# Kernel tuning notes

Hardware: AMD Instinct MI355X
Metric: run time of the kernel (lower is better)

Reference implementation:

```python
import jax, jax.numpy as jnp
import numpy as np

B, S, E, DK = 8, 2048, 1024, 64


def setup_inputs() -> dict:
    key = jax.random.key(0)
    ks = jax.random.split(key, 10)
    inv_e = 1.0 / np.sqrt(E)
    return {
        "k": jax.random.normal(ks[0], (B, S, E), dtype=jnp.float32),
        "q": jax.random.normal(ks[1], (B, S, E), dtype=jnp.float32),
        "v": jax.random.normal(ks[2], (B, S, E), dtype=jnp.float32),
        "mask": jax.random.randint(ks[3], (B, S, S), 0, 2, dtype=jnp.int32),
        "w_q": jax.random.uniform(ks[4], (DK, E), jnp.float32, -inv_e, inv_e),
        "b_q": jax.random.uniform(ks[5], (DK,), jnp.float32, -inv_e, inv_e),
        "w_k": jax.random.uniform(ks[6], (DK, E), jnp.float32, -inv_e, inv_e),
        "b_k": jax.random.uniform(ks[7], (DK,), jnp.float32, -inv_e, inv_e),
        "w_v": jax.random.uniform(ks[8], (DK, E), jnp.float32, -inv_e, inv_e),
        "b_v": jax.random.uniform(ks[9], (DK,), jnp.float32, -inv_e, inv_e),
    }


def reference(k, q, v, mask, w_q, b_q, w_k, b_k, w_v, b_v):
    # Linear projections: x @ W^T + b  -> [B, S, DK]
    K = jnp.einsum('bse,de->bsd', k, w_k) + b_k
    Q = jnp.einsum('bse,de->bsd', q, w_q) + b_q
    V = jnp.einsum('bse,de->bsd', v, w_v) + b_v
    scale = 1.0 / jnp.sqrt(jnp.asarray(DK, dtype=Q.dtype))
    scores = jnp.einsum('bqd,bkd->bqk', Q, K) * scale  # [B, S, S]
    scores = jnp.where(mask == 0, jnp.asarray(-1e9, scores.dtype), scores)
    attention_weights = jax.nn.softmax(scores, axis=2)
    attention_scores = jnp.einsum('bqk,bkd->bqd', attention_weights, V)
    return attention_scores, attention_weights
```

## Files before the change

### kernel.cpp

```cpp
#include <hip/hip_runtime.h>
#include <math.h>
#include <stdint.h>

#define BB 8
#define SS 2048
#define EE 1024
#define DKK 64

typedef _Float16 half8 __attribute__((ext_vector_type(8)));
typedef float floatx4 __attribute__((ext_vector_type(4)));

__device__ __forceinline__ half8 cvt8(float4 a, float4 b) {
  half8 h;
  h[0] = (_Float16)a.x; h[1] = (_Float16)a.y; h[2] = (_Float16)a.z; h[3] = (_Float16)a.w;
  h[4] = (_Float16)b.x; h[5] = (_Float16)b.y; h[6] = (_Float16)b.z; h[7] = (_Float16)b.w;
  return h;
}

__device__ __forceinline__ void split8(float4 a, float4 b, half8& hi, half8& lo) {
  float va[8] = {a.x, a.y, a.z, a.w, b.x, b.y, b.z, b.w};
#pragma unroll
  for (int j = 0; j < 8; ++j) {
    _Float16 h = (_Float16)va[j];
    hi[j] = h;
    lo[j] = (_Float16)(va[j] - (float)h);
  }
}

__global__ __launch_bounds__(256, 3) void proj_kernel(
    const float* __restrict__ q_in, const float* __restrict__ k_in,
    const float* __restrict__ v_in,
    const float* __restrict__ w_q, const float* __restrict__ b_q,
    const float* __restrict__ w_k, const float* __restrict__ b_k,
    const float* __restrict__ w_v, const float* __restrict__ b_v,
    float* __restrict__ Qp, float* __restrict__ Kp, float* __restrict__ VpT) {
  const int which = blockIdx.y;
  const float* X = which == 0 ? q_in : (which == 1 ? k_in : v_in);
  const float* W = which == 0 ? w_q : (which == 1 ? w_k : w_v);
  const float* bias = which == 0 ? b_q : (which == 1 ? b_k : b_v);

  __shared__ __align__(16) char Xh[64 * 128];
  __shared__ __align__(16) char Xl[64 * 128];
  __shared__ __align__(16) char Wh[64 * 128];
  __shared__ __align__(16) char Wl[64 * 128];

  const int t = threadIdx.x;
  const int row0 = blockIdx.x * 64;
  const int sr = t >> 2;
  const int c4 = t & 3;
  const int l = t & 63;
  const int li = l & 15, g = l >> 4;
  const int w = t >> 6;

  const float* xbase = X + (size_t)(row0 + sr) * EE + c4 * 16;
  const float* wbase = W + (size_t)sr * EE + c4 * 16;

  float4 xr[4], wr[4];
#pragma unroll
  for (int u = 0; u < 4; ++u) {
    xr[u] = ((const float4*)xbase)[u];
    wr[u] = ((const float4*)wbase)[u];
  }

  floatx4 acc[4];
#pragma unroll
  for (int c = 0; c < 4; ++c) acc[c] = (floatx4){0.f, 0.f, 0.f, 0.f};

  const int xrow_off = (w * 16 + li) * 128;
  const int swz = li & 7;

  for (int e0 = 0; e0 < EE; e0 += 64) {
    half8 xh0, xl0, xh1, xl1, wh0, wl0, wh1, wl1;
    split8(xr[0], xr[1], xh0, xl0);
    split8(xr[2], xr[3], xh1, xl1);
    split8(wr[0], wr[1], wh0, wl0);
    split8(wr[2], wr[3], wh1, wl1);
    __syncthreads();
    {
      const int p0 = ((c4 * 2 + 0) ^ (sr & 7)) * 16;
      const int p1 = ((c4 * 2 + 1) ^ (sr & 7)) * 16;
      *(half8*)(Xh + sr * 128 + p0) = xh0;
      *(half8*)(Xh + sr * 128 + p1) = xh1;
      *(half8*)(Xl + sr * 128 + p0) = xl0;
      *(half8*)(Xl + sr * 128 + p1) = xl1;
      *(half8*)(Wh + sr * 128 + p0) = wh0;
      *(half8*)(Wh + sr * 128 + p1) = wh1;
      *(half8*)(Wl + sr * 128 + p0) = wl0;
      *(half8*)(Wl + sr * 128 + p1) = wl1;
    }
    if (e0 + 64 < EE) {
#pragma unroll
      for (int u = 0; u < 4; ++u) {
        xr[u] = ((const float4*)(xbase + e0 + 64))[u];
        wr[u] = ((const float4*)(wbase + e0 + 64))[u];
      }
    }
    __syncthreads();
    half8 axh[2], axl[2];
#pragma unroll
    for (int h = 0; h < 2; ++h) {
      const int apos = ((h * 4 + g) ^ swz) * 16;
      axh[h] = *(const half8*)(Xh + xrow_off + apos);
      axl[h] = *(const half8*)(Xl + xrow_off + apos);
    }
#pragma unroll
    for (int c = 0; c < 4; ++c) {
      const int brow_off = (c * 16 + li) * 128;
#pragma unroll
      for (int h = 0; h < 2; ++h) {
        const int bpos = ((h * 4 + g) ^ swz) * 16;
        half8 bh = *(const half8*)(Wh + brow_off + bpos);
        half8 bl = *(const half8*)(Wl + brow_off + bpos);
        acc[c] = __builtin_amdgcn_mfma_f32_16x16x32_f16(axh[h], bh, acc[c], 0, 0, 0);
        acc[c] = __builtin_amdgcn_mfma_f32_16x16x32_f16(axh[h], bl, acc[c], 0, 0, 0);
        acc[c] = __builtin_amdgcn_mfma_f32_16x16x32_f16(axl[h], bh, acc[c], 0, 0, 0);
      }
    }
  }

  float bvv[4];
#pragma unroll
  for (int c = 0; c < 4; ++c) bvv[c] = bias[c * 16 + li];

  if (which < 2) {
    float* P = (which == 0) ? Qp : Kp;
#pragma unroll
    for (int c = 0; c < 4; ++c)
#pragma unroll
      for (int r = 0; r < 4; ++r)
        P[(size_t)(row0 + w * 16 + g * 4 + r) * DKK + c * 16 + li] = acc[c][r] + bvv[c];
  } else {
    const int bb = row0 >> 11;
    const int s0 = row0 & (SS - 1);
#pragma unroll
    for (int c = 0; c < 4; ++c)
#pragma unroll
      for (int r = 0; r < 4; ++r)
        VpT[((size_t)bb * DKK + c * 16 + li) * SS + s0 + w * 16 + g * 4 + r] =
            acc[c][r] + bvv[c];
  }
}

__global__ __launch_bounds__(512, 4) void attn_kernel(
    const float* __restrict__ Qp, const float* __restrict__ Kp,
    const float* __restrict__ VpT, const int* __restrict__ mask,
    float* __restrict__ outsc, float* __restrict__ wts) {
  __shared__ __align__(16) char Kraw[128 * 128];
  __shared__ __align__(16) char Vraw[64 * 256];
  __shared__ __align__(16) char Praw[2 * 16 * 272];
  __shared__ uint32_t mbits[512][5];
  __shared__ float mlb[2][4][16][2];

  const int t = threadIdx.x;
  const int b = blockIdx.x & 7;
  const int q0 = (blockIdx.x >> 3) * 32;
  const int l = t & 63;
  const int g = l >> 4, li = l & 15;
  const int w = t >> 6;
  const int qhalf = w & 1, cq = w >> 1;
  const float SCALE = 0.125f;

  half8 aq[2];
  {
    const float* qptr = Qp + ((size_t)b * SS + q0 + qhalf * 16 + li) * DKK;
#pragma unroll
    for (int h = 0; h < 2; ++h) {
      float4 a = *(const float4*)(qptr + h * 32 + g * 8);
      float4 c4 = *(const float4*)(qptr + h * 32 + g * 8 + 4);
      aq[h] = cvt8(a, c4);
    }
  }

  float m_r[4], l_r[4], rl_r[4];
#pragma unroll
  for (int r = 0; r < 4; ++r) { m_r[r] = -3.0e38f; l_r[r] = 0.f; }
#pragma unroll
  for (int i = 0; i < 4; ++i) mbits[t][i] = 0;

  const size_t qrow0 = (size_t)b * SS + q0 + qhalf * 16 + g * 4;

  for (int kt = 0; kt < 16; ++kt) {
    __syncthreads();
    {
      const int kr = t >> 3, c = t & 7;
#pragma unroll
      for (int p = 0; p < 2; ++p) {
        const int kk = kr + p * 64;
        const float* src = Kp + ((size_t)b * SS + (size_t)kt * 128 + kk) * DKK + c * 8;
        float4 a = ((const float4*)src)[0];
        float4 d4 = ((const float4*)src)[1];
        *(half8*)(Kraw + kk * 128 + ((c ^ (kk & 7)) * 16)) = cvt8(a, d4);
      }
    }
    __syncthreads();
    floatx4 sc[2];
#pragma unroll
    for (int cb2 = 0; cb2 < 2; ++cb2) {
      const int krow = (cq * 2 + cb2) * 16 + li;
      floatx4 acc = {0.f, 0.f, 0.f, 0.f};
#pragma unroll
      for (int h = 0; h < 2; ++h) {
        half8 bk = *(const half8*)(Kraw + krow * 128 + (((h * 4 + g) ^ (li & 7)) * 16));
        acc = __builtin_amdgcn_mfma_f32_16x16x32_f16(aq[h], bk, acc, 0, 0, 0);
      }
      sc[cb2] = acc;
    }
    uint32_t mbt = 0;
#pragma unroll
    for (int r = 0; r < 4; ++r) {
      float v0, v1;
      {
        const int kk = kt * 128 + (cq * 2 + 0) * 16 + li;
        const int mz = mask[(qrow0 + r) * SS + kk];
        v0 = mz ? sc[0][r] * SCALE : -1.0e9f;
        mbt |= (uint32_t)(mz != 0) << (0 + r);
      }
      {
        const int kk = kt * 128 + (cq * 2 + 1) * 16 + li;
        const int mz = mask[(qrow0 + r) * SS + kk];
        v1 = mz ? sc[1][r] * SCALE : -1.0e9f;
        mbt |= (uint32_t)(mz != 0) << (4 + r);
      }
      const float tmax = fmaxf(v0, v1);
      const float nm = fmaxf(m_r[r], tmax);
      l_r[r] = l_r[r] * __expf(m_r[r] - nm) + __expf(v0 - nm) + __expf(v1 - nm);
      m_r[r] = nm;
    }
    mbits[t][kt >> 2] |= mbt << ((kt & 3) * 8);
  }

#pragma unroll
  for (int off = 1; off < 16; off <<= 1) {
#pragma unroll
    for (int r = 0; r < 4; ++r) {
      const float om = __shfl_xor(m_r[r], off);
      const float ol = __shfl_xor(l_r[r], off);
      const float nm = fmaxf(m_r[r], om);
      l_r[r] = l_r[r] * __expf(m_r[r] - nm) + ol * __expf(om - nm);
      m_r[r] = nm;
    }
  }
  if (li == 0) {
#pragma unroll
    for (int r = 0; r < 4; ++r) {
      mlb[qhalf][cq][g * 4 + r][0] = m_r[r];
      mlb[qhalf][cq][g * 4 + r][1] = l_r[r];
    }
  }
  __syncthreads();
#pragma unroll
  for (int r = 0; r < 4; ++r) {
    float mm = -3.0e38f;
#pragma unroll
    for (int p = 0; p < 4; ++p) mm = fmaxf(mm, mlb[qhalf][p][g * 4 + r][0]);
    float ll = 0.f;
#pragma unroll
    for (int p = 0; p < 4; ++p)
      ll += mlb[qhalf][p][g * 4 + r][1] * __expf(mlb[qhalf][p][g * 4 + r][0] - mm);
    m_r[r] = mm;
    rl_r[r] = 1.f / ll;
  }

  floatx4 pacc = {0.f, 0.f, 0.f, 0.f};
  for (int kt = 0; kt < 16; ++kt) {
    __syncthreads();
    {
      const int kr = t >> 3, c = t & 7;
#pragma unroll
      for (int p = 0; p < 2; ++p) {
        const int kk = kr + p * 64;
        const float* src = Kp + ((size_t)b * SS + (size_t)kt * 128 + kk) * DKK + c * 8;
        float4 a = ((const float4*)src)[0];
        float4 d4 = ((const float4*)src)[1];
        *(half8*)(Kraw + kk * 128 + ((c ^ (kk & 7)) * 16)) = cvt8(a, d4);
      }
    }
    {
      const int dr = t >> 4, c = t & 15;
#pragma unroll
      for (int p = 0; p < 2; ++p) {
        const int d = dr + p * 32;
        const float* src = VpT + ((size_t)b * DKK + d) * SS + (size_t)kt * 128 + c * 8;
        float4 a = ((const float4*)src)[0];
        float4 e4 = ((const float4*)src)[1];
        *(half8*)(Vraw + d * 256 + ((c ^ (d & 7)) * 16)) = cvt8(a, e4);
      }
    }
    __syncthreads();
    floatx4 sc[2];
#pragma unroll
    for (int cb2 = 0; cb2 < 2; ++cb2) {
      const int krow = (cq * 2 + cb2) * 16 + li;
      floatx4 acc = {0.f, 0.f, 0.f, 0.f};
#pragma unroll
      for (int h = 0; h < 2; ++h) {
        half8 bk = *(const half8*)(Kraw + krow * 128 + (((h * 4 + g) ^ (li & 7)) * 16));
        acc = __builtin_amdgcn_mfma_f32_16x16x32_f16(aq[h], bk, acc, 0, 0, 0);
      }
      sc[cb2] = acc;
    }
    const uint32_t mbt = mbits[t][kt >> 2] >> ((kt & 3) * 8);
#pragma unroll
    for (int r = 0; r < 4; ++r) {
      const float mm = m_r[r], rl = rl_r[r];
#pragma unroll
      for (int cb2 = 0; cb2 < 2; ++cb2) {
        const int cb = cq * 2 + cb2;
        const int kk = kt * 128 + cb * 16 + li;
        const float s = ((mbt >> (cb2 * 4 + r)) & 1u) ? sc[cb2][r] * SCALE : -1.0e9f;
        const float wv = __expf(s - mm) * rl;
        wts[(qrow0 + r) * SS + kk] = wv;
        *(_Float16*)(Praw + qhalf * 4352 + (g * 4 + r) * 272 + (cb * 16 + li) * 2) =
            (_Float16)wv;
      }
    }
    __syncthreads();
#pragma unroll
    for (int kb = 0; kb < 4; ++kb) {
      const half8 ap = *(const half8*)(Praw + qhalf * 4352 + li * 272 + kb * 64 + g * 16);
      const int dd = cq * 16 + li;
      const half8 bv = *(const half8*)(Vraw + dd * 256 + (((kb * 4 + g) ^ (dd & 7)) * 16));
      pacc = __builtin_amdgcn_mfma_f32_16x16x32_f16(ap, bv, pacc, 0, 0, 0);
    }
  }
#pragma unroll
  for (int r = 0; r < 4; ++r) {
    outsc[(qrow0 + r) * DKK + cq * 16 + li] = pacc[r];
  }
}

extern "C" void kernel_launch(void* const* d_in, const int* in_sizes, int n_in,
                              void* d_out, int out_size, void* d_ws, size_t ws_size,
                              hipStream_t stream) {
  (void)in_sizes; (void)n_in; (void)out_size; (void)ws_size;
  const float* k_in = (const float*)d_in[0];
  const float* q_in = (const float*)d_in[1];
  const float* v_in = (const float*)d_in[2];
  const int* mask = (const int*)d_in[3];
  const float* w_q = (const float*)d_in[4];
  const float* b_q = (const float*)d_in[5];
  const float* w_k = (const float*)d_in[6];
  const float* b_k = (const float*)d_in[7];
  const float* w_v = (const float*)d_in[8];
  const float* b_v = (const float*)d_in[9];

  float* out_scores = (float*)d_out;
  float* out_weights = out_scores + (size_t)BB * SS * DKK;

  float* Qp = (float*)d_ws;
  float* Kp = Qp + (size_t)BB * SS * DKK;
  float* VpT = Kp + (size_t)BB * SS * DKK;

  proj_kernel<<<dim3(256, 3), 256, 0, stream>>>(q_in, k_in, v_in, w_q, b_q,
                                                w_k, b_k, w_v, b_v, Qp, Kp, VpT);
  attn_kernel<<<512, 512, 0, stream>>>(Qp, Kp, VpT, mask, out_scores, out_weights);
}
```

Baseline: 150.4 us.

## Split attention into flash pass and separate weights kernel with fp16 projections

Projections are now stored as fp16 instead of fp32, which halves workspace traffic and removes per-tile conversions. The two-pass attention kernel becomes a single-pass online-softmax flash kernel. It packs the mask into bits (stored both in shared memory and in global memory), accumulates O across waves and writes per-row max and normalizer statistics. A third kernel recomputes QK^T from the packed mask and stored statistics to write the full weights matrix. The intent is to stop reading the mask twice and to cut redundant work, at the cost of an extra launch and recomputing the scores.

```diff
diff --git a/kernel.cpp b/kernel.cpp
--- a/kernel.cpp
+++ b/kernel.cpp
@@ -9,13 +9,6 @@
 
 typedef _Float16 half8 __attribute__((ext_vector_type(8)));
 typedef float floatx4 __attribute__((ext_vector_type(4)));
-
-__device__ __forceinline__ half8 cvt8(float4 a, float4 b) {
-  half8 h;
-  h[0] = (_Float16)a.x; h[1] = (_Float16)a.y; h[2] = (_Float16)a.z; h[3] = (_Float16)a.w;
-  h[4] = (_Float16)b.x; h[5] = (_Float16)b.y; h[6] = (_Float16)b.z; h[7] = (_Float16)b.w;
-  return h;
-}
 
 __device__ __forceinline__ void split8(float4 a, float4 b, half8& hi, half8& lo) {
   float va[8] = {a.x, a.y, a.z, a.w, b.x, b.y, b.z, b.w};
@@ -33,7 +26,8 @@
     const float* __restrict__ w_q, const float* __restrict__ b_q,
     const float* __restrict__ w_k, const float* __restrict__ b_k,
     const float* __restrict__ w_v, const float* __restrict__ b_v,
-    float* __restrict__ Qp, float* __restrict__ Kp, float* __restrict__ VpT) {
+    _Float16* __restrict__ Qh, _Float16* __restrict__ Kh,
+    _Float16* __restrict__ VhT) {
   const int which = blockIdx.y;
   const float* X = which == 0 ? q_in : (which == 1 ? k_in : v_in);
   const float* W = which == 0 ? w_q : (which == 1 ? w_k : w_v);
@@ -123,12 +117,13 @@
   for (int c = 0; c < 4; ++c) bvv[c] = bias[c * 16 + li];
 
   if (which < 2) {
-    float* P = (which == 0) ? Qp : Kp;
+    _Float16* P = (which == 0) ? Qh : Kh;
 #pragma unroll
     for (int c = 0; c < 4; ++c)
 #pragma unroll
       for (int r = 0; r < 4; ++r)
-        P[(size_t)(row0 + w * 16 + g * 4 + r) * DKK + c * 16 + li] = acc[c][r] + bvv[c];
+        P[(size_t)(row0 + w * 16 + g * 4 + r) * DKK + c * 16 + li] =
+            (_Float16)(acc[c][r] + bvv[c]);
   } else {
     const int bb = row0 >> 11;
     const int s0 = row0 & (SS - 1);
@@ -136,196 +131,274 @@
     for (int c = 0; c < 4; ++c)
 #pragma unroll
       for (int r = 0; r < 4; ++r)
-        VpT[((size_t)bb * DKK + c * 16 + li) * SS + s0 + w * 16 + g * 4 + r] =
-            acc[c][r] + bvv[c];
+        VhT[((size_t)bb * DKK + c * 16 + li) * SS + s0 + w * 16 + g * 4 + r] =
+            (_Float16)(acc[c][r] + bvv[c]);
   }
 }
 
-__global__ __launch_bounds__(512, 4) void attn_kernel(
-    const float* __restrict__ Qp, const float* __restrict__ Kp,
-    const float* __restrict__ VpT, const int* __restrict__ mask,
-    float* __restrict__ outsc, float* __restrict__ wts) {
-  __shared__ __align__(16) char Kraw[128 * 128];
-  __shared__ __align__(16) char Vraw[64 * 256];
-  __shared__ __align__(16) char Praw[2 * 16 * 272];
-  __shared__ uint32_t mbits[512][5];
-  __shared__ float mlb[2][4][16][2];
+__global__ __launch_bounds__(512, 4) void flash_kernel(
+    const _Float16* __restrict__ Qh, const _Float16* __restrict__ Kh,
+    const _Float16* __restrict__ VhT, const int* __restrict__ mask,
+    float* __restrict__ outsc, uint32_t* __restrict__ mbits_g,
+    float* __restrict__ mstats) {
+  __shared__ __align__(16) char Klds[16384];
+  __shared__ __align__(16) char Vlds[16384];
+  __shared__ uint32_t mwords[32][66];
+  __shared__ float Obuf[32][68];
+  __shared__ float mlbuf[8][16][2];
+  __shared__ float lstat[32][2];
 
   const int t = threadIdx.x;
-  const int b = blockIdx.x & 7;
-  const int q0 = (blockIdx.x >> 3) * 32;
+  const int b = (int)blockIdx.x & 7;
+  const int q0 = ((int)blockIdx.x >> 3) * 32;
   const int l = t & 63;
-  const int g = l >> 4, li = l & 15;
+  const int li = l & 15, g = l >> 4;
   const int w = t >> 6;
-  const int qhalf = w & 1, cq = w >> 1;
+  const int qh = w & 1, ws = w >> 1;
   const float SCALE = 0.125f;
+
+  {
+    const int* mp = mask + ((size_t)b * SS + q0) * SS;
+    for (int j = 0; j < 128; ++j) {
+      const int flat = j * 512 + t;
+      const int mz = (mp[flat] != 0);
+      unsigned long long bal = __ballot(mz);
+      if ((l & 31) == 0) {
+        const uint32_t val = (uint32_t)(bal >> l);
+        const int word = flat >> 5;
+        const int qq = word >> 6, wc = word & 63;
+        mwords[qq][wc] = val;
+        mbits_g[((size_t)(b * SS + q0 + qq)) * 64 + wc] = val;
+      }
+    }
+  }
 
   half8 aq[2];
   {
-    const float* qptr = Qp + ((size_t)b * SS + q0 + qhalf * 16 + li) * DKK;
-#pragma unroll
-    for (int h = 0; h < 2; ++h) {
-      float4 a = *(const float4*)(qptr + h * 32 + g * 8);
-      float4 c4 = *(const float4*)(qptr + h * 32 + g * 8 + 4);
-      aq[h] = cvt8(a, c4);
-    }
-  }
-
-  float m_r[4], l_r[4], rl_r[4];
-#pragma unroll
-  for (int r = 0; r < 4; ++r) { m_r[r] = -3.0e38f; l_r[r] = 0.f; }
-#pragma unroll
-  for (int i = 0; i < 4; ++i) mbits[t][i] = 0;
-
-  const size_t qrow0 = (size_t)b * SS + q0 + qhalf * 16 + g * 4;
+    const _Float16* qp = Qh + ((size_t)b * SS + q0 + qh * 16 + li) * DKK;
+    aq[0] = *(const half8*)(qp + g * 8);
+    aq[1] = *(const half8*)(qp + 32 + g * 8);
+  }
+
+  float m_c = -3.0e38f, l_c = 0.f;
+  floatx4 O[4];
+#pragma unroll
+  for (int d = 0; d < 4; ++d) O[d] = (floatx4){0.f, 0.f, 0.f, 0.f};
+
+  __syncthreads();
 
   for (int kt = 0; kt < 16; ++kt) {
-    __syncthreads();
-    {
-      const int kr = t >> 3, c = t & 7;
-#pragma unroll
-      for (int p = 0; p < 2; ++p) {
-        const int kk = kr + p * 64;
-        const float* src = Kp + ((size_t)b * SS + (size_t)kt * 128 + kk) * DKK + c * 8;
-        float4 a = ((const float4*)src)[0];
-        float4 d4 = ((const float4*)src)[1];
-        *(half8*)(Kraw + kk * 128 + ((c ^ (kk & 7)) * 16)) = cvt8(a, d4);
-      }
-    }
-    __syncthreads();
+    half8 kv[2], vv[2];
+#pragma unroll
+    for (int p = 0; p < 2; ++p) {
+      const int slot = t + p * 512;
+      const int kr = slot >> 3, kc = slot & 7;
+      kv[p] = *(const half8*)(Kh + ((size_t)b * SS + kt * 128 + kr) * DKK +
+                              ((kc ^ (kr & 7)) * 8));
+      const int vd = slot >> 4, vc = slot & 15;
+      vv[p] = *(const half8*)(VhT + ((size_t)b * DKK + vd) * SS + kt * 128 +
+                              ((vc ^ (vd & 7)) * 8));
+    }
+    __syncthreads();
+#pragma unroll
+    for (int p = 0; p < 2; ++p) {
+      const int slot = t + p * 512;
+      *(half8*)(Klds + slot * 16) = kv[p];
+      *(half8*)(Vlds + slot * 16) = vv[p];
+    }
+    __syncthreads();
+
     floatx4 sc[2];
 #pragma unroll
-    for (int cb2 = 0; cb2 < 2; ++cb2) {
-      const int krow = (cq * 2 + cb2) * 16 + li;
+    for (int cb = 0; cb < 2; ++cb) {
+      const int krow = ws * 32 + cb * 16 + li;
+      const int rs = krow & 7;
       floatx4 acc = {0.f, 0.f, 0.f, 0.f};
 #pragma unroll
       for (int h = 0; h < 2; ++h) {
-        half8 bk = *(const half8*)(Kraw + krow * 128 + (((h * 4 + g) ^ (li & 7)) * 16));
-        acc = __builtin_amdgcn_mfma_f32_16x16x32_f16(aq[h], bk, acc, 0, 0, 0);
-      }
-      sc[cb2] = acc;
-    }
-    uint32_t mbt = 0;
-#pragma unroll
-    for (int r = 0; r < 4; ++r) {
-      float v0, v1;
-      {
-        const int kk = kt * 128 + (cq * 2 + 0) * 16 + li;
-        const int mz = mask[(qrow0 + r) * SS + kk];
-        v0 = mz ? sc[0][r] * SCALE : -1.0e9f;
-        mbt |= (uint32_t)(mz != 0) << (0 + r);
-      }
-      {
-        const int kk = kt * 128 + (cq * 2 + 1) * 16 + li;
-        const int mz = mask[(qrow0 + r) * SS + kk];
-        v1 = mz ? sc[1][r] * SCALE : -1.0e9f;
-        mbt |= (uint32_t)(mz != 0) << (4 + r);
-      }
-      const float tmax = fmaxf(v0, v1);
-      const float nm = fmaxf(m_r[r], tmax);
-      l_r[r] = l_r[r] * __expf(m_r[r] - nm) + __expf(v0 - nm) + __expf(v1 - nm);
-      m_r[r] = nm;
-    }
-    mbits[t][kt >> 2] |= mbt << ((kt & 3) * 8);
-  }
-
-#pragma unroll
-  for (int off = 1; off < 16; off <<= 1) {
-#pragma unroll
-    for (int r = 0; r < 4; ++r) {
-      const float om = __shfl_xor(m_r[r], off);
-      const float ol = __shfl_xor(l_r[r], off);
-      const float nm = fmaxf(m_r[r], om);
-      l_r[r] = l_r[r] * __expf(m_r[r] - nm) + ol * __expf(om - nm);
-      m_r[r] = nm;
-    }
-  }
-  if (li == 0) {
-#pragma unroll
-    for (int r = 0; r < 4; ++r) {
-      mlb[qhalf][cq][g * 4 + r][0] = m_r[r];
-      mlb[qhalf][cq][g * 4 + r][1] = l_r[r];
-    }
+        half8 ka = *(const half8*)(Klds + krow * 128 + (((h * 4 + g) ^ rs) * 16));
+        acc = __builtin_amdgcn_mfma_f32_16x16x32_f16(ka, aq[h], acc, 0, 0, 0);
+      }
+      sc[cb] = acc;
+    }
+
+    const uint32_t mw = mwords[qh * 16 + li][kt * 4 + ws];
+    float p[2][4];
+    float tmax = -3.0e38f;
+#pragma unroll
+    for (int cb = 0; cb < 2; ++cb)
+#pragma unroll
+      for (int r = 0; r < 4; ++r) {
+        const float s =
+            ((mw >> (cb * 16 + g * 4 + r)) & 1u) ? sc[cb][r] * SCALE : -1.0e9f;
+        p[cb][r] = s;
+        tmax = fmaxf(tmax, s);
+      }
+    tmax = fmaxf(tmax, __shfl_xor(tmax, 16));
+    tmax = fmaxf(tmax, __shfl_xor(tmax, 32));
+    const float m_new = fmaxf(m_c, tmax);
+    const float alpha = __expf(m_c - m_new);
+    m_c = m_new;
+    float lsum = 0.f;
+#pragma unroll
+    for (int cb = 0; cb < 2; ++cb)
+#pragma unroll
+      for (int r = 0; r < 4; ++r) {
+        p[cb][r] = __expf(p[cb][r] - m_new);
+        lsum += p[cb][r];
+      }
+    l_c = l_c * alpha + lsum;
+
+    half8 pB;
+#pragma unroll
+    for (int j = 0; j < 4; ++j) {
+      pB[j] = (_Float16)p[0][j];
+      pB[4 + j] = (_Float16)p[1][j];
+    }
+
+#pragma unroll
+    for (int dblk = 0; dblk < 4; ++dblk) {
+      const int d = dblk * 16 + li;
+      const int rowb = d * 256;
+      const int c1 = ws * 4 + (g >> 1);
+      const int c2 = c1 + 2;
+      const int sub = (g & 1) * 8;
+      uint2 a1 = *(const uint2*)(Vlds + rowb + ((c1 ^ (li & 7)) * 16) + sub);
+      uint2 a2 = *(const uint2*)(Vlds + rowb + ((c2 ^ (li & 7)) * 16) + sub);
+      half8 av;
+      *(uint2*)&av = a1;
+      *((uint2*)&av + 1) = a2;
+      O[dblk] = O[dblk] * alpha;
+      O[dblk] = __builtin_amdgcn_mfma_f32_16x16x32_f16(av, pB, O[dblk], 0, 0, 0);
+    }
+  }
+
+  l_c += __shfl_xor(l_c, 16);
+  l_c += __shfl_xor(l_c, 32);
+  if (g == 0) {
+    mlbuf[w][li][0] = m_c;
+    mlbuf[w][li][1] = l_c;
   }
   __syncthreads();
+  float mstar = -3.0e38f;
+#pragma unroll
+  for (int p2 = 0; p2 < 4; ++p2)
+    mstar = fmaxf(mstar, mlbuf[p2 * 2 + qh][li][0]);
+  float lstar = 0.f;
+#pragma unroll
+  for (int p2 = 0; p2 < 4; ++p2)
+    lstar += mlbuf[p2 * 2 + qh][li][1] * __expf(mlbuf[p2 * 2 + qh][li][0] - mstar);
+  const float fown = __expf(m_c - mstar);
+  if (g == 0 && ws == 0) {
+    lstat[qh * 16 + li][0] = mstar;
+    lstat[qh * 16 + li][1] = 1.f / lstar;
+  }
+#pragma unroll
+  for (int dblk = 0; dblk < 4; ++dblk) O[dblk] = O[dblk] * fown;
+
+  for (int ph = 0; ph < 4; ++ph) {
+    if (ws == ph) {
+      const int qq = qh * 16 + li;
+#pragma unroll
+      for (int dblk = 0; dblk < 4; ++dblk)
+#pragma unroll
+        for (int r = 0; r < 4; ++r) {
+          const int d = dblk * 16 + g * 4 + r;
+          if (ph == 0)
+            Obuf[qq][d] = O[dblk][r];
+          else
+            Obuf[qq][d] += O[dblk][r];
+        }
+    }
+    __syncthreads();
+  }
+
+  {
+    const int qq = t >> 4;
+    const int d0 = (t & 15) * 4;
+    const float rl = lstat[qq][1];
+    float4 o;
+    o.x = Obuf[qq][d0 + 0] * rl;
+    o.y = Obuf[qq][d0 + 1] * rl;
+    o.z = Obuf[qq][d0 + 2] * rl;
+    o.w = Obuf[qq][d0 + 3] * rl;
+    *(float4*)(outsc + ((size_t)(b * SS + q0 + qq)) * DKK + d0) = o;
+  }
+  if (t < 32) {
+    mstats[((size_t)(b * SS + q0 + t)) * 2 + 0] = lstat[t][0];
+    mstats[((size_t)(b * SS + q0 + t)) * 2 + 1] = lstat[t][1];
+  }
+}
+
+__global__ __launch_bounds__(512, 4) void weights_kernel(
+    const _Float16* __restrict__ Qh, const _Float16* __restrict__ Kh,
+    const uint32_t* __restrict__ mbits_g, const float* __restrict__ mstats,
+    float* __restrict__ wts) {
+  __shared__ __align__(16) char Klds[16384];
+
+  const int t = threadIdx.x;
+  const int b = (int)blockIdx.x & 7;
+  const int q0 = ((int)blockIdx.x >> 3) * 32;
+  const int l = t & 63;
+  const int li = l & 15, g = l >> 4;
+  const int w = t >> 6;
+  const int qh = w & 1, cq = w >> 1;
+  const float SCALE = 0.125f;
+
+  half8 aq[2];
+  {
+    const _Float16* qp = Qh + ((size_t)b * SS + q0 + qh * 16 + li) * DKK;
+    aq[0] = *(const half8*)(qp + g * 8);
+    aq[1] = *(const half8*)(qp + 32 + g * 8);
+  }
+  float mr[4], rl[4];
 #pragma unroll
   for (int r = 0; r < 4; ++r) {
-    float mm = -3.0e38f;
-#pragma unroll
-    for (int p = 0; p < 4; ++p) mm = fmaxf(mm, mlb[qhalf][p][g * 4 + r][0]);
-    float ll = 0.f;
-#pragma unroll
-    for (int p = 0; p < 4; ++p)
-      ll += mlb[qhalf][p][g * 4 + r][1] * __expf(mlb[qhalf][p][g * 4 + r][0] - mm);
-    m_r[r] = mm;
-    rl_r[r] = 1.f / ll;
-  }
-
-  floatx4 pacc = {0.f, 0.f, 0.f, 0.f};
+    const size_t q = (size_t)b * SS + q0 + qh * 16 + g * 4 + r;
+    mr[r] = mstats[q * 2 + 0];
+    rl[r] = mstats[q * 2 + 1];
+  }
+
   for (int kt = 0; kt < 16; ++kt) {
-    __syncthreads();
-    {
-      const int kr = t >> 3, c = t & 7;
-#pragma unroll
-      for (int p = 0; p < 2; ++p) {
-        const int kk = kr + p * 64;
-        const float* src = Kp + ((size_t)b * SS + (size_t)kt * 128 + kk) * DKK + c * 8;
-        float4 a = ((const float4*)src)[0];
-        float4 d4 = ((const float4*)src)[1];
-        *(half8*)(Kraw + kk * 128 + ((c ^ (kk & 7)) * 16)) = cvt8(a, d4);
-      }
-    }
-    {
-      const int dr = t >> 4, c = t & 15;
-#pragma unroll
-      for (int p = 0; p < 2; ++p) {
-        const int d = dr + p * 32;
-        const float* src = VpT + ((size_t)b * DKK + d) * SS + (size_t)kt * 128 + c * 8;
-        float4 a = ((const float4*)src)[0];
-        float4 e4 = ((const float4*)src)[1];
-        *(half8*)(Vraw + d * 256 + ((c ^ (d & 7)) * 16)) = cvt8(a, e4);
-      }
-    }
-    __syncthreads();
-    floatx4 sc[2];
-#pragma unroll
-    for (int cb2 = 0; cb2 < 2; ++cb2) {
-      const int krow = (cq * 2 + cb2) * 16 + li;
+    half8 kv[2];
+#pragma unroll
+    for (int p = 0; p < 2; ++p) {
+      const int slot = t + p * 512;
+      const int kr = slot >> 3, kc = slot & 7;
+      kv[p] = *(const half8*)(Kh + ((size_t)b * SS + kt * 128 + kr) * DKK +
+                              ((kc ^ (kr & 7)) * 8));
+    }
+    uint32_t mw[4];
+#pragma unroll
+    for (int r = 0; r < 4; ++r)
+      mw[r] = mbits_g[((size_t)(b * SS + q0 + qh * 16 + g * 4 + r)) * 64 +
+                      kt * 4 + cq];
+    __syncthreads();
+#pragma unroll
+    for (int p = 0; p < 2; ++p) {
+      const int slot = t + p * 512;
+      *(half8*)(Klds + slot * 16) = kv[p];
+    }
+    __syncthreads();
+#pragma unroll
+    for (int cb = 0; cb < 2; ++cb) {
+      const int krow = cq * 32 + cb * 16 + li;
+      const int rs = krow & 7;
       floatx4 acc = {0.f, 0.f, 0.f, 0.f};
 #pragma unroll
       for (int h = 0; h < 2; ++h) {
-        half8 bk = *(const half8*)(Kraw + krow * 128 + (((h * 4 + g) ^ (li & 7)) * 16));
-        acc = __builtin_amdgcn_mfma_f32_16x16x32_f16(aq[h], bk, acc, 0, 0, 0);
-      }
-      sc[cb2] = acc;
-    }
-    const uint32_t mbt = mbits[t][kt >> 2] >> ((kt & 3) * 8);
-#pragma unroll
-    for (int r = 0; r < 4; ++r) {
-      const float mm = m_r[r], rl = rl_r[r];
-#pragma unroll
-      for (int cb2 = 0; cb2 < 2; ++cb2) {
-        const int cb = cq * 2 + cb2;
-        const int kk = kt * 128 + cb * 16 + li;
-        const float s = ((mbt >> (cb2 * 4 + r)) & 1u) ? sc[cb2][r] * SCALE : -1.0e9f;
-        const float wv = __expf(s - mm) * rl;
-        wts[(qrow0 + r) * SS + kk] = wv;
-        *(_Float16*)(Praw + qhalf * 4352 + (g * 4 + r) * 272 + (cb * 16 + li) * 2) =
-            (_Float16)wv;
-      }
-    }
-    __syncthreads();
-#pragma unroll
-    for (int kb = 0; kb < 4; ++kb) {
-      const half8 ap = *(const half8*)(Praw + qhalf * 4352 + li * 272 + kb * 64 + g * 16);
-      const int dd = cq * 16 + li;
-      const half8 bv = *(const half8*)(Vraw + dd * 256 + (((kb * 4 + g) ^ (dd & 7)) * 16));
-      pacc = __builtin_amdgcn_mfma_f32_16x16x32_f16(ap, bv, pacc, 0, 0, 0);
-    }
-  }
-#pragma unroll
-  for (int r = 0; r < 4; ++r) {
-    outsc[(qrow0 + r) * DKK + cq * 16 + li] = pacc[r];
+        half8 kb = *(const half8*)(Klds + krow * 128 + (((h * 4 + g) ^ rs) * 16));
+        acc = __builtin_amdgcn_mfma_f32_16x16x32_f16(aq[h], kb, acc, 0, 0, 0);
+      }
+#pragma unroll
+      for (int r = 0; r < 4; ++r) {
+        const float wv = ((mw[r] >> (cb * 16 + li)) & 1u)
+                             ? __expf(acc[r] * SCALE - mr[r]) * rl[r]
+                             : 0.f;
+        wts[((size_t)(b * SS + q0 + qh * 16 + g * 4 + r)) * SS + kt * 128 +
+            cq * 32 + cb * 16 + li] = wv;
+      }
+    }
   }
 }
 
@@ -347,11 +420,17 @@
   float* out_scores = (float*)d_out;
   float* out_weights = out_scores + (size_t)BB * SS * DKK;
 
-  float* Qp = (float*)d_ws;
-  float* Kp = Qp + (size_t)BB * SS * DKK;
-  float* VpT = Kp + (size_t)BB * SS * DKK;
+  char* wsp = (char*)d_ws;
+  const size_t nBSD = (size_t)BB * SS * DKK;
+  _Float16* Qh = (_Float16*)wsp;
+  _Float16* Kh = (_Float16*)(wsp + nBSD * 2);
+  _Float16* VhT = (_Float16*)(wsp + nBSD * 4);
+  uint32_t* mbits_g = (uint32_t*)(wsp + nBSD * 6);
+  float* mstats = (float*)(wsp + nBSD * 6 + (size_t)BB * SS * 64 * 4);
 
   proj_kernel<<<dim3(256, 3), 256, 0, stream>>>(q_in, k_in, v_in, w_q, b_q,
-                                                w_k, b_k, w_v, b_v, Qp, Kp, VpT);
-  attn_kernel<<<512, 512, 0, stream>>>(Qp, Kp, VpT, mask, out_scores, out_weights);
+                                                w_k, b_k, w_v, b_v, Qh, Kh, VhT);
+  flash_kernel<<<512, 512, 0, stream>>>(Qh, Kh, VhT, mask, out_scores,
+                                        mbits_g, mstats);
+  weights_kernel<<<512, 512, 0, stream>>>(Qh, Kh, mbits_g, mstats, out_weights);
 }
```

New measurement: 187.4 us. 1.25x slower.
